# Kernel optimization log

Hardware: AMD Instinct MI355X
Metric: run time of the kernel (lower is better)

The kernel has to match this reference:

```python
import jax, jax.numpy as jnp
import numpy as np

N = 50000
E = 800000
DIN = 128
# SAGEConv layer dims: (in, out). conv0: input->embed; hidden: 128->64->128->256->512
DIMS = [(128, 128), (128, 64), (64, 128), (128, 256), (256, 512)]
NUM_CLASSES = 4


def setup_inputs() -> dict:
    key = jax.random.key(0)
    ks = jax.random.split(key, 3 * len(DIMS) + 4)
    inp = {"x": jax.random.normal(ks[0], (N, DIN), dtype=jnp.float32)}
    for i, (din, dout) in enumerate(DIMS):
        s = 1.0 / np.sqrt(din).astype(np.float32)
        inp[f"Wl{i}"] = jax.random.normal(ks[1 + 3 * i], (dout, din), dtype=jnp.float32) * s
        inp[f"bl{i}"] = jnp.zeros((dout,), dtype=jnp.float32)
        inp[f"Wr{i}"] = jax.random.normal(ks[2 + 3 * i], (dout, din), dtype=jnp.float32) * s
    dlast = DIMS[-1][1]
    inp["Wout"] = jax.random.normal(ks[-2], (NUM_CLASSES, dlast), dtype=jnp.float32) * (1.0 / np.sqrt(dlast).astype(np.float32))
    inp["bout"] = jnp.zeros((NUM_CLASSES,), dtype=jnp.float32)
    inp["edge_index"] = jax.random.randint(ks[-1], (2, E), 0, N, dtype=jnp.int32)
    return inp


def _forward(x, params, edge_index):
    src, dst = edge_index[0], edge_index[1]
    n = x.shape[0]
    # in-degree (count of incoming edges), clamped to >= 1 as in PyG mean aggregation
    deg = jax.ops.segment_sum(jnp.ones((src.shape[0],), x.dtype), dst, num_segments=n)
    deg_inv = (1.0 / jnp.maximum(deg, 1.0))[:, None]

    def sage(h, Wl, bl, Wr):
        # mean aggregation over incoming neighbors, then lin_l(agg) + lin_r(h)
        agg = jax.ops.segment_sum(h[src], dst, num_segments=n) * deg_inv
        return agg @ Wl.T + bl + h @ Wr.T

    h = x
    for i in range(len(DIMS)):
        h = jax.nn.relu(sage(h, params[f"Wl{i}"], params[f"bl{i}"], params[f"Wr{i}"]))
    logits = h @ params["Wout"].T + params["bout"]
    return jax.nn.softmax(logits, axis=-1)


def reference(x, Wl0, bl0, Wr0, Wl1, bl1, Wr1, Wl2, bl2, Wr2, Wl3, bl3, Wr3,
              Wl4, bl4, Wr4, Wout, bout, edge_index):
    params = {"Wl0": Wl0, "bl0": bl0, "Wr0": Wr0, "Wl1": Wl1, "bl1": bl1, "Wr1": Wr1,
              "Wl2": Wl2, "bl2": bl2, "Wr2": Wr2, "Wl3": Wl3, "bl3": bl3, "Wr3": Wr3,
              "Wl4": Wl4, "bl4": bl4, "Wr4": Wr4, "Wout": Wout, "bout": bout}
    return _forward(x, params, edge_index)
```

## Files before the change

kernel.cpp:

```cpp
#include <hip/hip_runtime.h>
#include <hip/hip_bf16.h>
#include <cstdint>
#include <cstddef>


typedef short bf16x8 __attribute__((ext_vector_type(8)));
typedef float f32x16 __attribute__((ext_vector_type(16)));

static inline int idiv_up(int a, int b) { return (a + b - 1) / b; }

static __device__ __forceinline__ float bf2f(unsigned short u) {
  union { unsigned int i; float f; } v; v.i = ((unsigned int)u) << 16; return v.f;
}
static __device__ __forceinline__ unsigned short f2bf(float f) {
  union { float f; unsigned int i; } v; v.f = f;
  return (unsigned short)((v.i + 0x7FFFu + ((v.i >> 16) & 1u)) >> 16);
}
static __device__ __forceinline__ float lo16(unsigned int u) { return bf2f((unsigned short)(u & 0xffffu)); }
static __device__ __forceinline__ float hi16(unsigned int u) { return bf2f((unsigned short)(u >> 16)); }
static __device__ __forceinline__ unsigned int packbf(float a, float b) {
  return (unsigned int)f2bf(a) | ((unsigned int)f2bf(b) << 16);
}

static __device__ __forceinline__ void gl_lds16(const void* g, void* l) {
  typedef __attribute__((address_space(3))) unsigned int lds_u32;
  typedef __attribute__((address_space(1))) const unsigned int glb_u32;
  __builtin_amdgcn_global_load_lds((glb_u32*)(uintptr_t)g,
                                   (lds_u32*)(unsigned int)(uintptr_t)l, 16, 0, 0);
}

__global__ void k_count_deg(const int* __restrict__ dst, int* __restrict__ deg, int E) {
  int e = blockIdx.x * blockDim.x + threadIdx.x;
  if (e < E) atomicAdd(deg + dst[e], 1);
}

__global__ __launch_bounds__(1024)
void k_scan(const int* __restrict__ deg, int* __restrict__ row_off, int* __restrict__ cursor,
            float* __restrict__ deg_inv, int n) {
  __shared__ int wsum[16];
  const int tid = threadIdx.x;
  const int lane = tid & 63, wid = tid >> 6;
  int carry = 0;
  for (int base = 0; base < n; base += 1024) {
    const int i = base + tid;
    const int v = (i < n) ? deg[i] : 0;
    int incl = v;
#pragma unroll
    for (int off = 1; off < 64; off <<= 1) {
      int t = __shfl_up(incl, off);
      if (lane >= off) incl += t;
    }
    if (lane == 63) wsum[wid] = incl;
    __syncthreads();
    if (wid == 0) {
      int wv = (lane < 16) ? wsum[lane] : 0;
#pragma unroll
      for (int off = 1; off < 16; off <<= 1) {
        int t = __shfl_up(wv, off);
        if (lane >= off) wv += t;
      }
      if (lane < 16) wsum[lane] = wv;
    }
    __syncthreads();
    const int woff = (wid > 0) ? wsum[wid - 1] : 0;
    if (i < n) {
      const int ro = carry + woff + incl - v;
      row_off[i] = ro;
      cursor[i] = ro;
      deg_inv[i] = 1.0f / (float)((v > 1) ? v : 1);
    }
    const int tot = wsum[15];
    __syncthreads();
    carry += tot;
  }
  if (tid == 0) row_off[n] = carry;
}

__global__ void k_fill_csr(const int* __restrict__ src, const int* __restrict__ dst,
                           int* __restrict__ cursor, int* __restrict__ esrc, int E) {
  int e = blockIdx.x * blockDim.x + threadIdx.x;
  if (e < E) {
    int d = dst[e];
    int p = atomicAdd(cursor + d, 1);
    esrc[p] = src[e];
  }
}

__global__ __launch_bounds__(256)
void k_conv_x(const float* __restrict__ src, unsigned short* __restrict__ dst, int n4) {
  for (int i = blockIdx.x * blockDim.x + threadIdx.x; i < n4; i += gridDim.x * blockDim.x) {
    const float4 v = *((const float4*)src + i);
    uint2 o;
    o.x = packbf(v.x, v.y);
    o.y = packbf(v.z, v.w);
    *((uint2*)dst + i) = o;
  }
}

struct PackJob { const float* src; unsigned short* dst; int O; int K; int colOff; int Opack; };
struct PackJobs { PackJob j[10]; };

__global__ __launch_bounds__(256)
void k_pack_w(PackJobs jobs) {
  const PackJob J = jobs.j[blockIdx.y];
  const int total = J.O * J.K / 2;
  for (int u = blockIdx.x * blockDim.x + threadIdx.x; u < total; u += gridDim.x * blockDim.x) {
    const int e = u * 2;
    const int col = e / J.K;
    const int k = e - col * J.K;
    const int kt = k >> 6, ch = (k >> 3) & 7, j = k & 7;
    const float f0 = J.src[(size_t)col * J.K + k];
    const float f1 = J.src[(size_t)col * J.K + k + 1];
    const int didx = kt * (J.Opack * 64) + ch * (J.Opack * 8) + (col + J.colOff) * 8 + j;
    ((unsigned int*)J.dst)[didx >> 1] = packbf(f0, f1);
  }
}

static __device__ __forceinline__ void acc_u4(float* acc, const uint4& v) {
  acc[0] += lo16(v.x); acc[1] += hi16(v.x);
  acc[2] += lo16(v.y); acc[3] += hi16(v.y);
  acc[4] += lo16(v.z); acc[5] += hi16(v.z);
  acc[6] += lo16(v.w); acc[7] += hi16(v.w);
}

__global__ __launch_bounds__(256)
void k_agg128(const unsigned short* __restrict__ h, const int* __restrict__ row_off,
              const int* __restrict__ esrc, const float* __restrict__ deg_inv,
              unsigned short* __restrict__ agg, int N) {
  const int node = blockIdx.x * 4 + (threadIdx.x >> 6);
  if (node >= N) return;
  const int lane = threadIdx.x & 63;
  const int g = lane >> 4, c = lane & 15;
  const int s0 = row_off[node], s1 = row_off[node + 1];
  const uint4* hp = (const uint4*)h;
  float acc[8] = {0.f, 0.f, 0.f, 0.f, 0.f, 0.f, 0.f, 0.f};
  for (int i = s0; i < s1; i += 16) {
    int el = i + (lane & 15);
    if (el >= s1) el = s1 - 1;
    const int ev = esrc[el];
    uint4 v[4];
#pragma unroll
    for (int u = 0; u < 4; ++u) {
      if (i + u * 4 < s1) {
        const int e = __shfl(ev, u * 4 + g);
        v[u] = hp[(size_t)e * 16 + c];
      }
    }
#pragma unroll
    for (int u = 0; u < 4; ++u)
      if (i + u * 4 + g < s1) acc_u4(acc, v[u]);
  }
#pragma unroll
  for (int j = 0; j < 8; ++j) {
    acc[j] += __shfl_xor(acc[j], 16);
    acc[j] += __shfl_xor(acc[j], 32);
  }
  if (g == 0) {
    const float di = deg_inv[node];
    uint4 o;
    o.x = packbf(acc[0] * di, acc[1] * di);
    o.y = packbf(acc[2] * di, acc[3] * di);
    o.z = packbf(acc[4] * di, acc[5] * di);
    o.w = packbf(acc[6] * di, acc[7] * di);
    ((uint4*)agg)[(size_t)node * 16 + c] = o;
  }
}

__global__ __launch_bounds__(256)
void k_agg256(const unsigned short* __restrict__ h, const int* __restrict__ row_off,
              const int* __restrict__ esrc, const float* __restrict__ deg_inv,
              unsigned short* __restrict__ agg, int N) {
  const int node = blockIdx.x * 4 + (threadIdx.x >> 6);
  if (node >= N) return;
  const int lane = threadIdx.x & 63;
  const int g = lane >> 5, c = lane & 31;
  const int s0 = row_off[node], s1 = row_off[node + 1];
  const uint4* hp = (const uint4*)h;
  float acc[8] = {0.f, 0.f, 0.f, 0.f, 0.f, 0.f, 0.f, 0.f};
  for (int i = s0; i < s1; i += 16) {
    int el = i + (lane & 15);
    if (el >= s1) el = s1 - 1;
    const int ev = esrc[el];
    uint4 v[8];
#pragma unroll
    for (int u = 0; u < 8; ++u) {
      if (i + u * 2 < s1) {
        const int e = __shfl(ev, u * 2 + g);
        v[u] = hp[(size_t)e * 32 + c];
      }
    }
#pragma unroll
    for (int u = 0; u < 8; ++u)
      if (i + u * 2 + g < s1) acc_u4(acc, v[u]);
  }
#pragma unroll
  for (int j = 0; j < 8; ++j) acc[j] += __shfl_xor(acc[j], 32);
  if (g == 0) {
    const float di = deg_inv[node];
    uint4 o;
    o.x = packbf(acc[0] * di, acc[1] * di);
    o.y = packbf(acc[2] * di, acc[3] * di);
    o.z = packbf(acc[4] * di, acc[5] * di);
    o.w = packbf(acc[6] * di, acc[7] * di);
    ((uint4*)agg)[(size_t)node * 32 + c] = o;
  }
}

__global__ __launch_bounds__(256)
void k_agg64(const unsigned short* __restrict__ h, const int* __restrict__ row_off,
             const int* __restrict__ esrc, const float* __restrict__ deg_inv,
             unsigned short* __restrict__ agg, int N) {
  const int node = blockIdx.x * 4 + (threadIdx.x >> 6);
  if (node >= N) return;
  const int lane = threadIdx.x & 63;
  const int g = lane >> 3, c = lane & 7;
  const int s0 = row_off[node], s1 = row_off[node + 1];
  const uint4* hp = (const uint4*)h;
  float acc[8] = {0.f, 0.f, 0.f, 0.f, 0.f, 0.f, 0.f, 0.f};
  for (int i = s0; i < s1; i += 16) {
    int el = i + (lane & 15);
    if (el >= s1) el = s1 - 1;
    const int ev = esrc[el];
    uint4 v[2];
#pragma unroll
    for (int u = 0; u < 2; ++u) {
      if (i + u * 8 < s1) {
        const int e = __shfl(ev, u * 8 + g);
        v[u] = hp[(size_t)e * 8 + c];
      }
    }
#pragma unroll
    for (int u = 0; u < 2; ++u)
      if (i + u * 8 + g < s1) acc_u4(acc, v[u]);
  }
#pragma unroll
  for (int j = 0; j < 8; ++j) {
    acc[j] += __shfl_xor(acc[j], 8);
    acc[j] += __shfl_xor(acc[j], 16);
    acc[j] += __shfl_xor(acc[j], 32);
  }
  if (g == 0) {
    const float di = deg_inv[node];
    uint4 o;
    o.x = packbf(acc[0] * di, acc[1] * di);
    o.y = packbf(acc[2] * di, acc[3] * di);
    o.z = packbf(acc[4] * di, acc[5] * di);
    o.w = packbf(acc[6] * di, acc[7] * di);
    ((uint4*)agg)[(size_t)node * 8 + c] = o;
  }
}

__global__ __launch_bounds__(256)
void k_agg_post64(const unsigned short* __restrict__ z, const int* __restrict__ row_off,
                  const int* __restrict__ esrc, const float* __restrict__ deg_inv,
                  const float* __restrict__ bias, unsigned short* __restrict__ out, int N) {
  const int node = blockIdx.x * 4 + (threadIdx.x >> 6);
  if (node >= N) return;
  const int lane = threadIdx.x & 63;
  const int g = lane >> 3, c = lane & 7;
  const int s0 = row_off[node], s1 = row_off[node + 1];
  const uint4* zp = (const uint4*)z;
  float acc[8] = {0.f, 0.f, 0.f, 0.f, 0.f, 0.f, 0.f, 0.f};
  for (int i = s0; i < s1; i += 16) {
    int el = i + (lane & 15);
    if (el >= s1) el = s1 - 1;
    const int ev = esrc[el];
    uint4 v[2];
#pragma unroll
    for (int u = 0; u < 2; ++u) {
      if (i + u * 8 < s1) {
        const int e = __shfl(ev, u * 8 + g);
        v[u] = zp[(size_t)e * 16 + c];
      }
    }
#pragma unroll
    for (int u = 0; u < 2; ++u)
      if (i + u * 8 + g < s1) acc_u4(acc, v[u]);
  }
#pragma unroll
  for (int j = 0; j < 8; ++j) {
    acc[j] += __shfl_xor(acc[j], 8);
    acc[j] += __shfl_xor(acc[j], 16);
    acc[j] += __shfl_xor(acc[j], 32);
  }
  if (g == 0) {
    const float di = deg_inv[node];
    const uint4 yr = zp[(size_t)node * 16 + 8 + c];
    float y[8];
    y[0] = lo16(yr.x); y[1] = hi16(yr.x); y[2] = lo16(yr.y); y[3] = hi16(yr.y);
    y[4] = lo16(yr.z); y[5] = hi16(yr.z); y[6] = lo16(yr.w); y[7] = hi16(yr.w);
    float r[8];
#pragma unroll
    for (int j = 0; j < 8; ++j)
      r[j] = fmaxf(acc[j] * di + y[j] + bias[c * 8 + j], 0.f);
    uint4 o;
    o.x = packbf(r[0], r[1]);
    o.y = packbf(r[2], r[3]);
    o.z = packbf(r[4], r[5]);
    o.w = packbf(r[6], r[7]);
    ((uint4*)out)[(size_t)node * 8 + c] = o;
  }
}

template <int WC, int NCB, bool FUSED>
__global__ __launch_bounds__(WC * 128)
void k_sage_gemm(const unsigned short* __restrict__ A0, const unsigned short* __restrict__ B0,
                 const unsigned short* __restrict__ A1, const unsigned short* __restrict__ B1,
                 const float* __restrict__ bias, unsigned short* __restrict__ C,
                 int Nn, int K, int O) {
  constexpr int BN = WC * 64;
  constexpr int T = WC * 128;
  constexpr int ACH = 1024;
  constexpr int BCH = BN * 8;
  constexpr int LPT = (ACH + BCH) / T;
  constexpr int BSH = (WC == 1) ? 6 : ((WC == 2) ? 7 : 8);
  constexpr int LDSBUF = 16384 + BN * 128;
  __shared__ char lds[2 * LDSBUF];

  const int nrp = (Nn + 127) >> 7;
  const int bid = blockIdx.x;
  const int r8 = bid & 7;
  const int tb = bid >> 3;
  const int cb = tb % NCB;
  const int rowp = (tb / NCB) * 8 + r8;
  if (rowp >= nrp) return;

  const int tid = threadIdx.x;
  const int w = tid >> 6, lane = tid & 63;
  const int wr = w / WC, wc = w % WC;
  const int fr = lane & 31, fq = lane >> 5;
  const int row0 = rowp * 128 + wr * 64;
  const int colb = cb * BN;

  const int KT0 = K >> 6;
  const int NT = FUSED ? 2 * KT0 : KT0;

  f32x16 acc[2][2];
#pragma unroll
  for (int m = 0; m < 2; ++m)
#pragma unroll
    for (int cn = 0; cn < 2; ++cn)
#pragma unroll
      for (int r = 0; r < 16; ++r) acc[m][cn][r] = 0.f;

  auto stage = [&](int buf, int t) {
    const unsigned short* Ab;
    const unsigned short* Bb;
    int ktl;
    if (FUSED) {
      const int ph = (t >= KT0) ? 1 : 0;
      Ab = ph ? A1 : A0;
      Bb = ph ? B1 : B0;
      ktl = t - ph * KT0;
    } else {
      Ab = A0; Bb = B0; ktl = t;
    }
    char* lb = lds + buf * LDSBUF;
#pragma unroll
    for (int i = 0; i < LPT; ++i) {
      const int ch = tid + i * T;
      if (ch < ACH) {
        const int ar = ch >> 3, s = ch & 7;
        int g = rowp * 128 + ar;
        if (g >= Nn) g = Nn - 1;
        gl_lds16(Ab + (size_t)g * K + ktl * 64 + ((s ^ (ar & 7)) << 3), lb + ch * 16);
      } else {
        const int cbch = ch - ACH;
        const int chunk = cbch >> BSH, colrel = cbch & (BN - 1);
        gl_lds16(Bb + (size_t)ktl * O * 64 + chunk * O * 8 + (colb + colrel) * 8,
                 lb + 16384 + cbch * 16);
      }
    }
  };

  stage(0, 0);
#pragma unroll 1
  for (int t = 0; t < NT; ++t) {
    asm volatile("s_waitcnt vmcnt(0)" ::: "memory");
    __syncthreads();
    if (t + 1 < NT) stage((t + 1) & 1, t + 1);
    const char* lb = lds + (t & 1) * LDSBUF;
#pragma unroll
    for (int k16i = 0; k16i < 4; ++k16i) {
      const int c = k16i * 2 + fq;
      bf16x8 af[2], bg[2];
#pragma unroll
      for (int m = 0; m < 2; ++m) {
        const int rl = wr * 64 + m * 32 + fr;
        af[m] = *(const bf16x8*)(lb + rl * 128 + ((c ^ (rl & 7)) << 4));
      }
#pragma unroll
      for (int cn = 0; cn < 2; ++cn) {
        const int colrel = wc * 64 + cn * 32 + fr;
        bg[cn] = *(const bf16x8*)(lb + 16384 + c * (BN * 16) + colrel * 16);
      }
#pragma unroll
      for (int m = 0; m < 2; ++m)
#pragma unroll
        for (int cn = 0; cn < 2; ++cn)
          acc[m][cn] = __builtin_amdgcn_mfma_f32_32x32x16_bf16(af[m], bg[cn], acc[m][cn], 0, 0, 0);
    }
  }

#pragma unroll
  for (int cn = 0; cn < 2; ++cn) {
    const int col = colb + wc * 64 + cn * 32 + fr;
    float bb = 0.f;
    if (FUSED) bb = bias[col];
#pragma unroll
    for (int m = 0; m < 2; ++m) {
#pragma unroll
      for (int reg = 0; reg < 16; ++reg) {
        float v = acc[m][cn][reg];
        if (FUSED) v = fmaxf(v + bb, 0.f);
        const float nb = __shfl_xor(v, 1);
        const int row = row0 + m * 32 + (reg & 3) + 8 * (reg >> 2) + 4 * fq;
        if (!(lane & 1) && row < Nn) {
          *(unsigned int*)(C + (size_t)row * O + col) = packbf(v, nb);
        }
      }
    }
  }
}

__global__ __launch_bounds__(256)
void k_out_softmax(const unsigned short* __restrict__ h, const float* __restrict__ W4,
                   const float* __restrict__ b, float* __restrict__ out, int N) {
  const int n = blockIdx.x * 4 + (threadIdx.x >> 6);
  if (n >= N) return;
  const int lane = threadIdx.x & 63;
  const unsigned int* hp = (const unsigned int*)h + (size_t)n * 256;
  float a[4] = {0.f, 0.f, 0.f, 0.f};
#pragma unroll
  for (int it = 0; it < 4; ++it) {
    const unsigned int v = hp[it * 64 + lane];
    const float lo = lo16(v);
    const float hi = hi16(v);
    const int k = (it * 64 + lane) * 2;
#pragma unroll
    for (int c = 0; c < 4; ++c)
      a[c] += lo * W4[c * 512 + k] + hi * W4[c * 512 + k + 1];
  }
#pragma unroll
  for (int off = 32; off > 0; off >>= 1) {
#pragma unroll
    for (int c = 0; c < 4; ++c) a[c] += __shfl_down(a[c], off);
  }
  if (lane == 0) {
    const float l0 = a[0] + b[0], l1 = a[1] + b[1], l2 = a[2] + b[2], l3 = a[3] + b[3];
    const float m = fmaxf(fmaxf(l0, l1), fmaxf(l2, l3));
    const float e0 = expf(l0 - m), e1 = expf(l1 - m), e2 = expf(l2 - m), e3 = expf(l3 - m);
    const float inv = 1.0f / (e0 + e1 + e2 + e3);
    float4 r; r.x = e0 * inv; r.y = e1 * inv; r.z = e2 * inv; r.w = e3 * inv;
    *(float4*)(out + (size_t)n * 4) = r;
  }
}

extern "C" void kernel_launch(void* const* d_in, const int* in_sizes, int n_in,
                              void* d_out, int out_size, void* d_ws, size_t ws_size,
                              hipStream_t stream) {
  const float* x = (const float*)d_in[0];
  const float* Wl[5] = {(const float*)d_in[1], (const float*)d_in[4], (const float*)d_in[7],
                        (const float*)d_in[10], (const float*)d_in[13]};
  const float* bl[5] = {(const float*)d_in[2], (const float*)d_in[5], (const float*)d_in[8],
                        (const float*)d_in[11], (const float*)d_in[14]};
  const float* Wr[5] = {(const float*)d_in[3], (const float*)d_in[6], (const float*)d_in[9],
                        (const float*)d_in[12], (const float*)d_in[15]};
  const float* Wout = (const float*)d_in[16];
  const float* bout = (const float*)d_in[17];
  const int* eidx = (const int*)d_in[18];

  const int N = in_sizes[0] / 128;
  const int E = in_sizes[18] / 2;
  const int* srcI = eidx;
  const int* dstI = eidx + E;

  const int Kd[5] = {128, 128, 64, 128, 256};
  const int Od[5] = {128, 64, 128, 256, 512};

  char* ws = (char*)d_ws;
  size_t p = 0;
  auto alloc = [&](size_t bytes) { size_t r = p; p += (bytes + 255) & ~(size_t)255; return r; };
  int*   deg     = (int*)(ws + alloc((size_t)N * 4));
  int*   row_off = (int*)(ws + alloc((size_t)(N + 1) * 4));
  int*   cursor  = (int*)(ws + alloc((size_t)N * 4));
  float* deg_inv = (float*)(ws + alloc((size_t)N * 4));
  int*   esrc    = (int*)(ws + alloc((size_t)E * 4));
  unsigned short* xb = (unsigned short*)(ws + alloc((size_t)N * 128 * 2));
  unsigned short* wlb[5];
  unsigned short* wrb[5];
  for (int l = 0; l < 5; ++l) {
    wlb[l] = (unsigned short*)(ws + alloc((size_t)Od[l] * Kd[l] * 2));
    wrb[l] = (unsigned short*)(ws + alloc((size_t)Od[l] * Kd[l] * 2));
  }
  unsigned short* wcat1 = (unsigned short*)(ws + alloc((size_t)128 * 128 * 2));
  unsigned short* bufA = (unsigned short*)(ws + alloc((size_t)N * 512 * 2));
  unsigned short* bufB = (unsigned short*)(ws + alloc((size_t)N * 256 * 2));
  unsigned short* agg  = (unsigned short*)(ws + alloc((size_t)N * 256 * 2));
  (void)ws_size; (void)n_in; (void)out_size;

  k_conv_x<<<128, 256, 0, stream>>>(x, xb, N * 128 / 4);
  PackJobs jobs;
  for (int l = 0; l < 5; ++l) {
    if (l == 1) {
      jobs.j[2] = {Wl[1], wcat1, 64, 128, 0, 128};
      jobs.j[3] = {Wr[1], wcat1, 64, 128, 64, 128};
    } else {
      jobs.j[2 * l]     = {Wl[l], wlb[l], Od[l], Kd[l], 0, Od[l]};
      jobs.j[2 * l + 1] = {Wr[l], wrb[l], Od[l], Kd[l], 0, Od[l]};
    }
  }
  k_pack_w<<<dim3(32, 10), 256, 0, stream>>>(jobs);

  hipMemsetAsync(deg, 0, (size_t)N * 4, stream);
  k_count_deg<<<idiv_up(E, 256), 256, 0, stream>>>(dstI, deg, E);
  k_scan<<<1, 1024, 0, stream>>>(deg, row_off, cursor, deg_inv, N);
  k_fill_csr<<<idiv_up(E, 256), 256, 0, stream>>>(srcI, dstI, cursor, esrc, E);

  const int gx8 = 8 * ((idiv_up(N, 128) + 7) / 8);

  k_agg128<<<idiv_up(N, 4), 256, 0, stream>>>(xb, row_off, esrc, deg_inv, agg, N);
  k_sage_gemm<2, 1, true><<<gx8, 256, 0, stream>>>(agg, wlb[0], xb, wrb[0], bl[0], bufA, N, 128, 128);

  k_sage_gemm<2, 1, false><<<gx8, 256, 0, stream>>>(bufA, wcat1, bufA, wcat1, bl[1], agg, N, 128, 128);
  k_agg_post64<<<idiv_up(N, 4), 256, 0, stream>>>(agg, row_off, esrc, deg_inv, bl[1], bufB, N);

  k_agg64<<<idiv_up(N, 4), 256, 0, stream>>>(bufB, row_off, esrc, deg_inv, agg, N);
  k_sage_gemm<2, 1, true><<<gx8, 256, 0, stream>>>(agg, wlb[2], bufB, wrb[2], bl[2], bufA, N, 64, 128);

  k_agg128<<<idiv_up(N, 4), 256, 0, stream>>>(bufA, row_off, esrc, deg_inv, agg, N);
  k_sage_gemm<2, 2, true><<<2 * gx8, 256, 0, stream>>>(agg, wlb[3], bufA, wrb[3], bl[3], bufB, N, 128, 256);

  k_agg256<<<idiv_up(N, 4), 256, 0, stream>>>(bufB, row_off, esrc, deg_inv, agg, N);
  k_sage_gemm<2, 4, true><<<4 * gx8, 256, 0, stream>>>(agg, wlb[4], bufB, wrb[4], bl[4], bufA, N, 256, 512);

  k_out_softmax<<<idiv_up(N, 4), 256, 0, stream>>>(bufA, Wout, bout, (float*)d_out, N);
}
```

Measured before the change: 461.9 us.

## Parallelize degree scan across blocks and read GEMM B operand directly from global

```diff
diff --git a/kernel.cpp b/kernel.cpp
--- a/kernel.cpp
+++ b/kernel.cpp
@@ -35,45 +35,77 @@
 }
 
 __global__ __launch_bounds__(1024)
-void k_scan(const int* __restrict__ deg, int* __restrict__ row_off, int* __restrict__ cursor,
-            float* __restrict__ deg_inv, int n) {
+void k_scan1(const int* __restrict__ deg, int* __restrict__ loc, int* __restrict__ part, int n) {
   __shared__ int wsum[16];
   const int tid = threadIdx.x;
   const int lane = tid & 63, wid = tid >> 6;
-  int carry = 0;
-  for (int base = 0; base < n; base += 1024) {
-    const int i = base + tid;
-    const int v = (i < n) ? deg[i] : 0;
-    int incl = v;
-#pragma unroll
-    for (int off = 1; off < 64; off <<= 1) {
-      int t = __shfl_up(incl, off);
-      if (lane >= off) incl += t;
-    }
-    if (lane == 63) wsum[wid] = incl;
-    __syncthreads();
-    if (wid == 0) {
-      int wv = (lane < 16) ? wsum[lane] : 0;
-#pragma unroll
-      for (int off = 1; off < 16; off <<= 1) {
-        int t = __shfl_up(wv, off);
-        if (lane >= off) wv += t;
-      }
-      if (lane < 16) wsum[lane] = wv;
-    }
-    __syncthreads();
-    const int woff = (wid > 0) ? wsum[wid - 1] : 0;
-    if (i < n) {
-      const int ro = carry + woff + incl - v;
-      row_off[i] = ro;
-      cursor[i] = ro;
-      deg_inv[i] = 1.0f / (float)((v > 1) ? v : 1);
-    }
-    const int tot = wsum[15];
-    __syncthreads();
-    carry += tot;
-  }
-  if (tid == 0) row_off[n] = carry;
+  const int i = blockIdx.x * 1024 + tid;
+  const int v = (i < n) ? deg[i] : 0;
+  int incl = v;
+#pragma unroll
+  for (int off = 1; off < 64; off <<= 1) {
+    int t = __shfl_up(incl, off);
+    if (lane >= off) incl += t;
+  }
+  if (lane == 63) wsum[wid] = incl;
+  __syncthreads();
+  if (wid == 0) {
+    int wv = (lane < 16) ? wsum[lane] : 0;
+#pragma unroll
+    for (int off = 1; off < 16; off <<= 1) {
+      int t = __shfl_up(wv, off);
+      if (lane >= off) wv += t;
+    }
+    if (lane < 16) wsum[lane] = wv;
+  }
+  __syncthreads();
+  const int woff = (wid > 0) ? wsum[wid - 1] : 0;
+  if (i < n) loc[i] = woff + incl;
+  if (tid == 1023) part[blockIdx.x] = woff + incl;
+}
+
+__global__ __launch_bounds__(1024)
+void k_scan2(int* __restrict__ part, int nb) {
+  __shared__ int wsum[16];
+  const int tid = threadIdx.x;
+  const int lane = tid & 63, wid = tid >> 6;
+  const int v = (tid < nb) ? part[tid] : 0;
+  int incl = v;
+#pragma unroll
+  for (int off = 1; off < 64; off <<= 1) {
+    int t = __shfl_up(incl, off);
+    if (lane >= off) incl += t;
+  }
+  if (lane == 63) wsum[wid] = incl;
+  __syncthreads();
+  if (wid == 0) {
+    int wv = (lane < 16) ? wsum[lane] : 0;
+#pragma unroll
+    for (int off = 1; off < 16; off <<= 1) {
+      int t = __shfl_up(wv, off);
+      if (lane >= off) wv += t;
+    }
+    if (lane < 16) wsum[lane] = wv;
+  }
+  __syncthreads();
+  const int woff = (wid > 0) ? wsum[wid - 1] : 0;
+  if (tid < nb) part[tid] = woff + incl - v;
+  if (tid == 0) part[nb] = wsum[15];
+}
+
+__global__ __launch_bounds__(256)
+void k_scan3(const int* __restrict__ deg, const int* __restrict__ loc, const int* __restrict__ part,
+             int* __restrict__ row_off, int* __restrict__ cursor, float* __restrict__ deg_inv,
+             int n, int nb) {
+  const int i = blockIdx.x * blockDim.x + threadIdx.x;
+  if (i < n) {
+    const int v = deg[i];
+    const int ro = part[i >> 10] + loc[i] - v;
+    row_off[i] = ro;
+    cursor[i] = ro;
+    deg_inv[i] = 1.0f / (float)((v > 1) ? v : 1);
+  }
+  if (i == 0) row_off[n] = part[nb];
 }
 
 __global__ void k_fill_csr(const int* __restrict__ src, const int* __restrict__ dst,
@@ -311,11 +343,8 @@
   constexpr int BN = WC * 64;
   constexpr int T = WC * 128;
   constexpr int ACH = 1024;
-  constexpr int BCH = BN * 8;
-  constexpr int LPT = (ACH + BCH) / T;
-  constexpr int BSH = (WC == 1) ? 6 : ((WC == 2) ? 7 : 8);
-  constexpr int LDSBUF = 16384 + BN * 128;
-  __shared__ char lds[2 * LDSBUF];
+  constexpr int LPT = ACH / T;
+  __shared__ char lds[2 * 16384];
 
   const int nrp = (Nn + 127) >> 7;
   const int bid = blockIdx.x;
@@ -345,31 +374,22 @@
 
   auto stage = [&](int buf, int t) {
     const unsigned short* Ab;
-    const unsigned short* Bb;
     int ktl;
     if (FUSED) {
       const int ph = (t >= KT0) ? 1 : 0;
       Ab = ph ? A1 : A0;
-      Bb = ph ? B1 : B0;
       ktl = t - ph * KT0;
     } else {
-      Ab = A0; Bb = B0; ktl = t;
-    }
-    char* lb = lds + buf * LDSBUF;
+      Ab = A0; ktl = t;
+    }
+    char* lb = lds + buf * 16384;
 #pragma unroll
     for (int i = 0; i < LPT; ++i) {
       const int ch = tid + i * T;
-      if (ch < ACH) {
-        const int ar = ch >> 3, s = ch & 7;
-        int g = rowp * 128 + ar;
-        if (g >= Nn) g = Nn - 1;
-        gl_lds16(Ab + (size_t)g * K + ktl * 64 + ((s ^ (ar & 7)) << 3), lb + ch * 16);
-      } else {
-        const int cbch = ch - ACH;
-        const int chunk = cbch >> BSH, colrel = cbch & (BN - 1);
-        gl_lds16(Bb + (size_t)ktl * O * 64 + chunk * O * 8 + (colb + colrel) * 8,
-                 lb + 16384 + cbch * 16);
-      }
+      const int ar = ch >> 3, s = ch & 7;
+      int g = rowp * 128 + ar;
+      if (g >= Nn) g = Nn - 1;
+      gl_lds16(Ab + (size_t)g * K + ktl * 64 + ((s ^ (ar & 7)) << 3), lb + ch * 16);
     }
   };
 
@@ -379,7 +399,17 @@
     asm volatile("s_waitcnt vmcnt(0)" ::: "memory");
     __syncthreads();
     if (t + 1 < NT) stage((t + 1) & 1, t + 1);
-    const char* lb = lds + (t & 1) * LDSBUF;
+    const char* lb = lds + (t & 1) * 16384;
+    const unsigned short* Bp;
+    int ktl;
+    if (FUSED) {
+      const int ph = (t >= KT0) ? 1 : 0;
+      Bp = ph ? B1 : B0;
+      ktl = t - ph * KT0;
+    } else {
+      Bp = B0; ktl = t;
+    }
+    const unsigned short* Bbase = Bp + (size_t)ktl * (O * 64) + (size_t)(colb + wc * 64) * 8;
 #pragma unroll
     for (int k16i = 0; k16i < 4; ++k16i) {
       const int c = k16i * 2 + fq;
@@ -390,10 +420,8 @@
         af[m] = *(const bf16x8*)(lb + rl * 128 + ((c ^ (rl & 7)) << 4));
       }
 #pragma unroll
-      for (int cn = 0; cn < 2; ++cn) {
-        const int colrel = wc * 64 + cn * 32 + fr;
-        bg[cn] = *(const bf16x8*)(lb + 16384 + c * (BN * 16) + colrel * 16);
-      }
+      for (int cn = 0; cn < 2; ++cn)
+        bg[cn] = *(const bf16x8*)(Bbase + (size_t)c * (O * 8) + (cn * 32 + fr) * 8);
 #pragma unroll
       for (int m = 0; m < 2; ++m)
 #pragma unroll
@@ -485,6 +513,8 @@
   int*   row_off = (int*)(ws + alloc((size_t)(N + 1) * 4));
   int*   cursor  = (int*)(ws + alloc((size_t)N * 4));
   float* deg_inv = (float*)(ws + alloc((size_t)N * 4));
+  int*   loc     = (int*)(ws + alloc((size_t)N * 4));
+  int*   part    = (int*)(ws + alloc((size_t)1032 * 4));
   int*   esrc    = (int*)(ws + alloc((size_t)E * 4));
   unsigned short* xb = (unsigned short*)(ws + alloc((size_t)N * 128 * 2));
   unsigned short* wlb[5];
@@ -514,7 +544,10 @@
 
   hipMemsetAsync(deg, 0, (size_t)N * 4, stream);
   k_count_deg<<<idiv_up(E, 256), 256, 0, stream>>>(dstI, deg, E);
-  k_scan<<<1, 1024, 0, stream>>>(deg, row_off, cursor, deg_inv, N);
+  const int nb = idiv_up(N, 1024);
+  k_scan1<<<nb, 1024, 0, stream>>>(deg, loc, part, N);
+  k_scan2<<<1, 1024, 0, stream>>>(part, nb);
+  k_scan3<<<idiv_up(N + 1, 256), 256, 0, stream>>>(deg, loc, part, row_off, cursor, deg_inv, N, nb);
   k_fill_csr<<<idiv_up(E, 256), 256, 0, stream>>>(srcI, dstI, cursor, esrc, E);
 
   const int gx8 = 8 * ((idiv_up(N, 128) + 7) / 8);
```

Result: faster. 414.9 us (-10.2%).
